# Optimization experiments

Measured on AMD Instinct MI355X. Metric: run time of the kernel, lower is better.

The kernel has to match this reference:

```python
import jax, jax.numpy as jnp
import numpy as np

B, L, D, V = 512, 128, 512, 100000

def setup_inputs() -> dict:
    key = jax.random.key(0)
    ks = jax.random.split(key, 8)
    return {
        "t1s": jax.random.randint(ks[0], (B,), 0, V),
        "t2s": jax.random.randint(ks[1], (B,), 0, V),
        "t1_contexts": jax.random.randint(ks[2], (B, L), 0, V),
        "t2_contexts": jax.random.randint(ks[3], (B, L), 0, V),
        "embed_table": jax.random.normal(ks[4], (V, D), dtype=jnp.float32),
        "att_mat": jax.random.normal(ks[5], (D, D), dtype=jnp.float32) * (6.0 / (D + D)) ** 0.5,
        "w_pred": jax.random.normal(ks[6], (D, 1), dtype=jnp.float32) * 0.02,
        "b_pred": jnp.zeros((1,), dtype=jnp.float32),
    }

def _frob_normalize(x):
    # torch.norm(mat, p=2) is the Frobenius norm of the whole (L, D) matrix
    n = jnp.sqrt(jnp.sum(x * x, axis=(1, 2), keepdims=True))
    return x / n

def reference(t1s, t2s, t1_contexts, t2_contexts, embed_table, att_mat, w_pred, b_pred):
    # dropout is identity in eval mode; t1s/t2s embeddings are unused in the
    # 'dynamic' branch (dead code in the original forward).
    A = _frob_normalize(embed_table[t1_contexts])  # (B, L, D)
    Bm = _frob_normalize(embed_table[t2_contexts])  # (B, L, D)
    # batched bilinear attention: tanh(A @ att_mat @ B^T)
    S = jnp.tanh(jnp.einsum('bld,de,bme->blm', A, att_mat, Bm))  # (B, L, L)
    rows = jax.nn.softmax(jnp.mean(S, axis=2), axis=1)  # (B, L)
    cols = jax.nn.softmax(jnp.mean(S, axis=1), axis=1)  # (B, L)
    newA = jnp.einsum('bld,bl->bd', A, rows)   # (B, D)
    newB = jnp.einsum('bld,bl->bd', Bm, cols)  # (B, D)
    logits = ((newA * newB) @ w_pred + b_pred).reshape(-1)  # (B,)
    return logits, S
```

## Files before the change

kernel.cpp:

```cpp
#include <hip/hip_runtime.h>
#include <hip/hip_bf16.h>
#include <stdint.h>

#define NB 512
#define NL 128
#define ND 512

typedef __bf16 bf16;
typedef __bf16 bf16x8 __attribute__((ext_vector_type(8)));
typedef float  f32x4  __attribute__((ext_vector_type(4)));

__global__ __launch_bounds__(256) void k_gather(const int* __restrict__ ctx1,
                                                const int* __restrict__ ctx2,
                                                const float* __restrict__ table,
                                                bf16* __restrict__ d1,
                                                bf16* __restrict__ d2,
                                                float* __restrict__ ss,
                                                const float* __restrict__ att,
                                                bf16* __restrict__ attT) {
    const int b = blockIdx.x, side = blockIdx.y, zc = blockIdx.z, t = threadIdx.x;
    if (side == 2) {
        int chunk = b * 8 + zc;
        if (chunk < 1024) {
            int i = chunk * 256 + t;
            int n = i >> 9, k = i & 511;
            attT[i] = (bf16)att[k * 512 + n];
        }
        return;
    }
    const int* __restrict__ ctx = side ? ctx2 : ctx1;
    bf16* __restrict__ dst = side ? d2 : d1;
    const int base = b * NL;
    const int dv = t & 127, lr = t >> 7;
    float acc = 0.f;
    #pragma unroll
    for (int i = 0; i < 8; ++i) {
        int l = zc * 16 + i * 2 + lr;
        int idx = ctx[base + l];
        float4 v = ((const float4*)table)[(size_t)idx * (ND / 4) + dv];
        acc += v.x * v.x + v.y * v.y + v.z * v.z + v.w * v.w;
        union { bf16 h[4]; uint2 u; } pk;
        pk.h[0] = (bf16)v.x; pk.h[1] = (bf16)v.y;
        pk.h[2] = (bf16)v.z; pk.h[3] = (bf16)v.w;
        *((uint2*)(dst + (size_t)(base + l) * ND) + dv) = pk.u;
    }
    for (int o = 32; o; o >>= 1) acc += __shfl_xor(acc, o);
    __shared__ float red[4];
    if ((t & 63) == 0) red[t >> 6] = acc;
    __syncthreads();
    if (t == 0) atomicAdd(&ss[side * NB + b], red[0] + red[1] + red[2] + red[3]);
}

__global__ __launch_bounds__(512) void k_fused(
        const bf16* __restrict__ Ab, const bf16* __restrict__ attT,
        const bf16* __restrict__ Bb, float* __restrict__ Sout,
        const float* __restrict__ ss,
        const float* __restrict__ w_pred, const float* __restrict__ b_pred,
        float* __restrict__ logits) {
    const int b = blockIdx.x;
    const int row0 = b * NL;
    const int tid = threadIdx.x;
    const int lane = tid & 63, w = tid >> 6;
    const int lm = lane & 15, quad = lane >> 4;

    __shared__ __align__(16) char smem[147456];
    bf16* Tls = (bf16*)smem;
    bf16* stA = (bf16*)smem;
    bf16* stT = (bf16*)(smem + 16384);
    bf16* Bst = (bf16*)(smem + 131072);
    float* pA = (float*)smem;
    float* pB = (float*)(smem + 16384);
    float* rowb = (float*)(smem + 131072);
    float* colb = (float*)(smem + 131072 + 2048);
    float* wrow = (float*)(smem + 131072 + 3072);
    float* wcol = (float*)(smem + 131072 + 3584);

    const int wm1 = (w & 1) * 64;
    const int wn1 = (w >> 1) * 128;
    f32x4 acc1[4][8] = {};

    for (int k0 = 0; k0 < ND; k0 += 64) {
        #pragma unroll
        for (int i = 0; i < 2; ++i) {
            int s = i * 512 + tid;
            int r = s >> 3, c = (s & 7) ^ (r & 7);
            __builtin_amdgcn_global_load_lds(
                (const __attribute__((address_space(1))) void*)(Ab + (size_t)(row0 + r) * ND + k0 + c * 8),
                (__attribute__((address_space(3))) void*)(stA + (size_t)(i * 512 + w * 64) * 8),
                16, 0, 0);
        }
        #pragma unroll
        for (int i = 0; i < 8; ++i) {
            int s = i * 512 + tid;
            int r = s >> 3, c = (s & 7) ^ (r & 7);
            __builtin_amdgcn_global_load_lds(
                (const __attribute__((address_space(1))) void*)(attT + (size_t)r * ND + k0 + c * 8),
                (__attribute__((address_space(3))) void*)(stT + (size_t)(i * 512 + w * 64) * 8),
                16, 0, 0);
        }
        __syncthreads();
        #pragma unroll
        for (int kk = 0; kk < 2; ++kk) {
            bf16x8 af[4], bfm[8];
            const int ca = (kk * 4 + quad) ^ (lm & 7);
            #pragma unroll
            for (int t4 = 0; t4 < 4; ++t4)
                af[t4] = *(const bf16x8*)&stA[(wm1 + t4 * 16 + lm) * 64 + ca * 8];
            #pragma unroll
            for (int t8 = 0; t8 < 8; ++t8)
                bfm[t8] = *(const bf16x8*)&stT[(wn1 + t8 * 16 + lm) * 64 + ca * 8];
            #pragma unroll
            for (int im = 0; im < 4; ++im)
                #pragma unroll
                for (int jn = 0; jn < 8; ++jn)
                    acc1[im][jn] = __builtin_amdgcn_mfma_f32_16x16x32_bf16(
                        af[im], bfm[jn], acc1[im][jn], 0, 0, 0);
        }
        __syncthreads();
    }

    #pragma unroll
    for (int im = 0; im < 4; ++im)
    #pragma unroll
    for (int jn = 0; jn < 8; ++jn)
    #pragma unroll
    for (int p = 0; p < 4; ++p) {
        int m = wm1 + im * 16 + quad * 4 + p;
        int n = wn1 + jn * 16 + lm;
        int ks = n >> 6, c = n & 63;
        int pos = (((c >> 3) ^ (m & 7)) << 3) + (c & 7);
        Tls[ks * 8192 + m * 64 + pos] = (bf16)acc1[im][jn][p];
    }
    __syncthreads();

    const int wm2 = (w & 1) * 64;
    const int wn2 = (w >> 1) * 32;
    f32x4 acc2[4][2] = {};

    for (int k0 = 0; k0 < ND; k0 += 64) {
        #pragma unroll
        for (int i = 0; i < 2; ++i) {
            int s = i * 512 + tid;
            int r = s >> 3, c = (s & 7) ^ (r & 7);
            __builtin_amdgcn_global_load_lds(
                (const __attribute__((address_space(1))) void*)(Bb + (size_t)(row0 + r) * ND + k0 + c * 8),
                (__attribute__((address_space(3))) void*)(Bst + (size_t)(i * 512 + w * 64) * 8),
                16, 0, 0);
        }
        __syncthreads();
        const bf16* Tk = Tls + (k0 >> 6) * 8192;
        #pragma unroll
        for (int kk = 0; kk < 2; ++kk) {
            bf16x8 af[4], bf2[2];
            const int ca = (kk * 4 + quad) ^ (lm & 7);
            #pragma unroll
            for (int t4 = 0; t4 < 4; ++t4)
                af[t4] = *(const bf16x8*)&Tk[(wm2 + t4 * 16 + lm) * 64 + ca * 8];
            #pragma unroll
            for (int t2 = 0; t2 < 2; ++t2)
                bf2[t2] = *(const bf16x8*)&Bst[(wn2 + t2 * 16 + lm) * 64 + ca * 8];
            #pragma unroll
            for (int im = 0; im < 4; ++im)
                #pragma unroll
                for (int jn = 0; jn < 2; ++jn)
                    acc2[im][jn] = __builtin_amdgcn_mfma_f32_16x16x32_bf16(
                        af[im], bf2[jn], acc2[im][jn], 0, 0, 0);
        }
        __syncthreads();
    }

    const float sc = rsqrtf(ss[b] * ss[NB + b]);
    float* __restrict__ Sb = Sout + (size_t)b * NL * NL;
    #pragma unroll
    for (int im = 0; im < 4; ++im)
    #pragma unroll
    for (int jn = 0; jn < 2; ++jn)
    #pragma unroll
    for (int p = 0; p < 4; ++p) {
        float v = tanhf(acc2[im][jn][p] * sc);
        acc2[im][jn][p] = v;
        int m = wm2 + im * 16 + quad * 4 + p;
        int n = wn2 + jn * 16 + lm;
        __builtin_nontemporal_store(v, &Sb[m * NL + n]);
    }
    #pragma unroll
    for (int im = 0; im < 4; ++im)
    #pragma unroll
    for (int p = 0; p < 4; ++p) {
        float r = acc2[im][0][p] + acc2[im][1][p];
        r += __shfl_xor(r, 1); r += __shfl_xor(r, 2);
        r += __shfl_xor(r, 4); r += __shfl_xor(r, 8);
        if (lm == 0) rowb[(w >> 1) * NL + wm2 + im * 16 + quad * 4 + p] = r;
    }
    #pragma unroll
    for (int jn = 0; jn < 2; ++jn) {
        float cv = 0.f;
        #pragma unroll
        for (int im = 0; im < 4; ++im)
            #pragma unroll
            for (int p = 0; p < 4; ++p) cv += acc2[im][jn][p];
        cv += __shfl_xor(cv, 16); cv += __shfl_xor(cv, 32);
        if (quad == 0) colb[(w & 1) * NL + wn2 + jn * 16 + lm] = cv;
    }
    __syncthreads();

    if (tid < 64) {
        float a  = (rowb[0 * NL + tid] + rowb[1 * NL + tid] + rowb[2 * NL + tid] + rowb[3 * NL + tid]) * (1.f / NL);
        float c2 = (rowb[0 * NL + tid + 64] + rowb[1 * NL + tid + 64] + rowb[2 * NL + tid + 64] + rowb[3 * NL + tid + 64]) * (1.f / NL);
        float mx = fmaxf(a, c2);
        for (int o = 32; o; o >>= 1) mx = fmaxf(mx, __shfl_xor(mx, o));
        float e0 = expf(a - mx), e1 = expf(c2 - mx);
        float s = e0 + e1;
        for (int o = 32; o; o >>= 1) s += __shfl_xor(s, o);
        float inv = 1.f / s;
        wrow[tid] = e0 * inv; wrow[tid + 64] = e1 * inv;
    } else if (tid < 128) {
        int q = tid - 64;
        float a  = (colb[0 * NL + q] + colb[1 * NL + q]) * (1.f / NL);
        float c2 = (colb[0 * NL + q + 64] + colb[1 * NL + q + 64]) * (1.f / NL);
        float mx = fmaxf(a, c2);
        for (int o = 32; o; o >>= 1) mx = fmaxf(mx, __shfl_xor(mx, o));
        float e0 = expf(a - mx), e1 = expf(c2 - mx);
        float s = e0 + e1;
        for (int o = 32; o; o >>= 1) s += __shfl_xor(s, o);
        float inv = 1.f / s;
        wcol[q] = e0 * inv; wcol[q + 64] = e1 * inv;
    }
    __syncthreads();

    const int c = tid & 63, g = tid >> 6;
    const bf16* __restrict__ Abase = Ab + (size_t)b * NL * ND;
    const bf16* __restrict__ Bbase = Bb + (size_t)b * NL * ND;
    float aacc[8] = {}, bacc[8] = {};
    for (int l = g; l < NL; l += 8) {
        float wr = wrow[l], wc = wcol[l];
        bf16x8 va = *(const bf16x8*)(Abase + (size_t)l * ND + c * 8);
        bf16x8 vb = *(const bf16x8*)(Bbase + (size_t)l * ND + c * 8);
        #pragma unroll
        for (int j = 0; j < 8; ++j) {
            aacc[j] += wr * (float)va[j];
            bacc[j] += wc * (float)vb[j];
        }
    }
    #pragma unroll
    for (int j = 0; j < 8; ++j) {
        pA[g * ND + c * 8 + j] = aacc[j];
        pB[g * ND + c * 8 + j] = bacc[j];
    }
    __syncthreads();

    if (tid < 64) {
        float dot = 0.f;
        #pragma unroll
        for (int j = 0; j < 8; ++j) {
            int d = tid * 8 + j;
            float na = 0.f, nb = 0.f;
            #pragma unroll
            for (int g2 = 0; g2 < 8; ++g2) {
                na += pA[g2 * ND + d];
                nb += pB[g2 * ND + d];
            }
            dot += na * nb * w_pred[d];
        }
        for (int o = 32; o; o >>= 1) dot += __shfl_xor(dot, o);
        if (tid == 0)
            logits[b] = dot * rsqrtf(ss[b]) * rsqrtf(ss[NB + b]) + b_pred[0];
    }
}

extern "C" void kernel_launch(void* const* d_in, const int* in_sizes, int n_in,
                              void* d_out, int out_size, void* d_ws, size_t ws_size,
                              hipStream_t stream) {
    const int*   t1c = (const int*)d_in[2];
    const int*   t2c = (const int*)d_in[3];
    const float* emb = (const float*)d_in[4];
    const float* att = (const float*)d_in[5];
    const float* wp  = (const float*)d_in[6];
    const float* bp  = (const float*)d_in[7];

    float* out    = (float*)d_out;
    float* logits = out;
    float* S      = out + NB;

    char* ws = (char*)d_ws;
    bf16*  Ab   = (bf16*)(ws);
    bf16*  Bb   = (bf16*)(ws + 67108864);
    bf16*  attT = (bf16*)(ws + 134217728);
    float* ss   = (float*)(ws + 134742016);

    hipMemsetAsync(ss, 0, 4096, stream);
    k_gather<<<dim3(NB, 3, 8), 256, 0, stream>>>(t1c, t2c, emb, Ab, Bb, ss, att, attT);
    k_fused<<<dim3(NB), 512, 0, stream>>>(Ab, attT, Bb, S, ss, wp, bp, logits);
}
```

Before: 411.8 us.

## Double-buffer GEMM stages with k=32 tiles and prefetch gather indices

Result: no change. 406.8 us (-1.2%).

```diff
diff --git a/kernel.cpp b/kernel.cpp
--- a/kernel.cpp
+++ b/kernel.cpp
@@ -9,6 +9,10 @@
 typedef __bf16 bf16;
 typedef __bf16 bf16x8 __attribute__((ext_vector_type(8)));
 typedef float  f32x4  __attribute__((ext_vector_type(4)));
+
+#define GLDS(src, dst) __builtin_amdgcn_global_load_lds( \
+    (const __attribute__((address_space(1))) void*)(src), \
+    (__attribute__((address_space(3))) void*)(dst), 16, 0, 0)
 
 __global__ __launch_bounds__(256) void k_gather(const int* __restrict__ ctx1,
                                                 const int* __restrict__ ctx2,
@@ -32,12 +36,14 @@
     bf16* __restrict__ dst = side ? d2 : d1;
     const int base = b * NL;
     const int dv = t & 127, lr = t >> 7;
+    int idxs[8];
+    #pragma unroll
+    for (int i = 0; i < 8; ++i) idxs[i] = ctx[base + zc * 16 + i * 2 + lr];
     float acc = 0.f;
     #pragma unroll
     for (int i = 0; i < 8; ++i) {
         int l = zc * 16 + i * 2 + lr;
-        int idx = ctx[base + l];
-        float4 v = ((const float4*)table)[(size_t)idx * (ND / 4) + dv];
+        float4 v = ((const float4*)table)[(size_t)idxs[i] * (ND / 4) + dv];
         acc += v.x * v.x + v.y * v.y + v.z * v.z + v.w * v.w;
         union { bf16 h[4]; uint2 u; } pk;
         pk.h[0] = (bf16)v.x; pk.h[1] = (bf16)v.y;
@@ -63,59 +69,64 @@
     const int lane = tid & 63, w = tid >> 6;
     const int lm = lane & 15, quad = lane >> 4;
 
-    __shared__ __align__(16) char smem[147456];
+    __shared__ __align__(16) char smem[151552];
+    bf16* sA0 = (bf16*)smem;
+    bf16* sT0 = (bf16*)(smem + 8192);
+    bf16* sA1 = (bf16*)(smem + 40960);
+    bf16* sT1 = (bf16*)(smem + 49152);
     bf16* Tls = (bf16*)smem;
-    bf16* stA = (bf16*)smem;
-    bf16* stT = (bf16*)(smem + 16384);
-    bf16* Bst = (bf16*)(smem + 131072);
+    bf16* sB0 = (bf16*)(smem + 131072);
+    bf16* sB1 = (bf16*)(smem + 139264);
     float* pA = (float*)smem;
     float* pB = (float*)(smem + 16384);
-    float* rowb = (float*)(smem + 131072);
-    float* colb = (float*)(smem + 131072 + 2048);
-    float* wrow = (float*)(smem + 131072 + 3072);
-    float* wcol = (float*)(smem + 131072 + 3584);
+    float* rowb = (float*)(smem + 147456);
+    float* colb = (float*)(smem + 147456 + 2048);
+    float* wrow = (float*)(smem + 147456 + 3072);
+    float* wcol = (float*)(smem + 147456 + 3584);
 
     const int wm1 = (w & 1) * 64;
     const int wn1 = (w >> 1) * 128;
     f32x4 acc1[4][8] = {};
 
-    for (int k0 = 0; k0 < ND; k0 += 64) {
-        #pragma unroll
-        for (int i = 0; i < 2; ++i) {
-            int s = i * 512 + tid;
-            int r = s >> 3, c = (s & 7) ^ (r & 7);
-            __builtin_amdgcn_global_load_lds(
-                (const __attribute__((address_space(1))) void*)(Ab + (size_t)(row0 + r) * ND + k0 + c * 8),
-                (__attribute__((address_space(3))) void*)(stA + (size_t)(i * 512 + w * 64) * 8),
-                16, 0, 0);
-        }
-        #pragma unroll
-        for (int i = 0; i < 8; ++i) {
-            int s = i * 512 + tid;
-            int r = s >> 3, c = (s & 7) ^ (r & 7);
-            __builtin_amdgcn_global_load_lds(
-                (const __attribute__((address_space(1))) void*)(attT + (size_t)r * ND + k0 + c * 8),
-                (__attribute__((address_space(3))) void*)(stT + (size_t)(i * 512 + w * 64) * 8),
-                16, 0, 0);
-        }
-        __syncthreads();
-        #pragma unroll
-        for (int kk = 0; kk < 2; ++kk) {
-            bf16x8 af[4], bfm[8];
-            const int ca = (kk * 4 + quad) ^ (lm & 7);
-            #pragma unroll
-            for (int t4 = 0; t4 < 4; ++t4)
-                af[t4] = *(const bf16x8*)&stA[(wm1 + t4 * 16 + lm) * 64 + ca * 8];
-            #pragma unroll
-            for (int t8 = 0; t8 < 8; ++t8)
-                bfm[t8] = *(const bf16x8*)&stT[(wn1 + t8 * 16 + lm) * 64 + ca * 8];
-            #pragma unroll
-            for (int im = 0; im < 4; ++im)
-                #pragma unroll
-                for (int jn = 0; jn < 8; ++jn)
-                    acc1[im][jn] = __builtin_amdgcn_mfma_f32_16x16x32_bf16(
-                        af[im], bfm[jn], acc1[im][jn], 0, 0, 0);
-        }
+    const int rA = tid >> 2, cA = tid & 3;
+
+    GLDS(Ab + (size_t)(row0 + rA) * ND + 0 + cA * 8, sA0 + tid * 8);
+    #pragma unroll
+    for (int i = 0; i < 4; ++i) {
+        int s = i * 512 + tid, r = s >> 2, c = s & 3;
+        GLDS(attT + (size_t)r * ND + 0 + c * 8, sT0 + s * 8);
+    }
+    __syncthreads();
+
+    for (int t = 0; t < 16; ++t) {
+        if (t < 15) {
+            const int k0 = (t + 1) * 32;
+            bf16* dA = (t & 1) ? sA0 : sA1;
+            bf16* dT = (t & 1) ? sT0 : sT1;
+            GLDS(Ab + (size_t)(row0 + rA) * ND + k0 + cA * 8, dA + tid * 8);
+            #pragma unroll
+            for (int i = 0; i < 4; ++i) {
+                int s = i * 512 + tid, r = s >> 2, c = s & 3;
+                GLDS(attT + (size_t)r * ND + k0 + c * 8, dT + s * 8);
+            }
+        } else {
+            GLDS(Bb + (size_t)(row0 + rA) * ND + 0 + cA * 8, sB0 + tid * 8);
+        }
+        const bf16* A_ = (t & 1) ? sA1 : sA0;
+        const bf16* T_ = (t & 1) ? sT1 : sT0;
+        bf16x8 af[4], bfm[8];
+        #pragma unroll
+        for (int t4 = 0; t4 < 4; ++t4)
+            af[t4] = *(const bf16x8*)&A_[(wm1 + t4 * 16 + lm) * 32 + quad * 8];
+        #pragma unroll
+        for (int t8 = 0; t8 < 8; ++t8)
+            bfm[t8] = *(const bf16x8*)&T_[(wn1 + t8 * 16 + lm) * 32 + quad * 8];
+        #pragma unroll
+        for (int im = 0; im < 4; ++im)
+            #pragma unroll
+            for (int jn = 0; jn < 8; ++jn)
+                acc1[im][jn] = __builtin_amdgcn_mfma_f32_16x16x32_bf16(
+                    af[im], bfm[jn], acc1[im][jn], 0, 0, 0);
         __syncthreads();
     }
 
@@ -127,9 +138,9 @@
     for (int p = 0; p < 4; ++p) {
         int m = wm1 + im * 16 + quad * 4 + p;
         int n = wn1 + jn * 16 + lm;
-        int ks = n >> 6, c = n & 63;
-        int pos = (((c >> 3) ^ (m & 7)) << 3) + (c & 7);
-        Tls[ks * 8192 + m * 64 + pos] = (bf16)acc1[im][jn][p];
+        int ks = n >> 5, kq = (n >> 3) & 3, e = n & 7;
+        int pos = kq ^ ((m >> 2) & 3);
+        Tls[ks * 4096 + m * 32 + pos * 8 + e] = (bf16)acc1[im][jn][p];
     }
     __syncthreads();
 
@@ -137,35 +148,27 @@
     const int wn2 = (w >> 1) * 32;
     f32x4 acc2[4][2] = {};
 
-    for (int k0 = 0; k0 < ND; k0 += 64) {
-        #pragma unroll
-        for (int i = 0; i < 2; ++i) {
-            int s = i * 512 + tid;
-            int r = s >> 3, c = (s & 7) ^ (r & 7);
-            __builtin_amdgcn_global_load_lds(
-                (const __attribute__((address_space(1))) void*)(Bb + (size_t)(row0 + r) * ND + k0 + c * 8),
-                (__attribute__((address_space(3))) void*)(Bst + (size_t)(i * 512 + w * 64) * 8),
-                16, 0, 0);
-        }
-        __syncthreads();
-        const bf16* Tk = Tls + (k0 >> 6) * 8192;
-        #pragma unroll
-        for (int kk = 0; kk < 2; ++kk) {
-            bf16x8 af[4], bf2[2];
-            const int ca = (kk * 4 + quad) ^ (lm & 7);
-            #pragma unroll
-            for (int t4 = 0; t4 < 4; ++t4)
-                af[t4] = *(const bf16x8*)&Tk[(wm2 + t4 * 16 + lm) * 64 + ca * 8];
-            #pragma unroll
-            for (int t2 = 0; t2 < 2; ++t2)
-                bf2[t2] = *(const bf16x8*)&Bst[(wn2 + t2 * 16 + lm) * 64 + ca * 8];
-            #pragma unroll
-            for (int im = 0; im < 4; ++im)
-                #pragma unroll
-                for (int jn = 0; jn < 2; ++jn)
-                    acc2[im][jn] = __builtin_amdgcn_mfma_f32_16x16x32_bf16(
-                        af[im], bf2[jn], acc2[im][jn], 0, 0, 0);
-        }
+    for (int t = 0; t < 16; ++t) {
+        if (t < 15) {
+            bf16* dB = (t & 1) ? sB0 : sB1;
+            GLDS(Bb + (size_t)(row0 + rA) * ND + (t + 1) * 32 + cA * 8, dB + tid * 8);
+        }
+        const bf16* B_ = (t & 1) ? sB1 : sB0;
+        bf16x8 af[4], bf2[2];
+        #pragma unroll
+        for (int t4 = 0; t4 < 4; ++t4) {
+            int r = wm2 + t4 * 16 + lm;
+            af[t4] = *(const bf16x8*)&Tls[t * 4096 + r * 32 + ((quad ^ ((r >> 2) & 3))) * 8];
+        }
+        #pragma unroll
+        for (int t2 = 0; t2 < 2; ++t2)
+            bf2[t2] = *(const bf16x8*)&B_[(wn2 + t2 * 16 + lm) * 32 + quad * 8];
+        #pragma unroll
+        for (int im = 0; im < 4; ++im)
+            #pragma unroll
+            for (int jn = 0; jn < 2; ++jn)
+                acc2[im][jn] = __builtin_amdgcn_mfma_f32_16x16x32_bf16(
+                    af[im], bf2[jn], acc2[im][jn], 0, 0, 0);
         __syncthreads();
     }
 
```
